# Kernel optimization log

Hardware: AMD Instinct MI355X
Metric: run time of the kernel (lower is better)

Reference implementation:

```python
import jax, jax.numpy as jnp
import numpy as np

ATT_UNITS = 64
DEC_DIM = 512
ENC_DIM = 512


def setup_inputs() -> dict:
    key = jax.random.key(0)
    k1, k2, k3, k4, k5 = jax.random.split(key, 5)
    B, S = 256, 512
    # glorot-uniform-ish init scales
    def glorot(k, shape):
        fan_in, fan_out = shape[0], shape[1]
        lim = np.sqrt(6.0 / (fan_in + fan_out))
        return jax.random.uniform(k, shape, jnp.float32, -lim, lim)
    return {
        "decoder_hidden_state": jax.random.normal(k1, (B, DEC_DIM), jnp.float32),
        "encoder_output": jax.random.normal(k2, (B, S, ENC_DIM), jnp.float32),
        "w1_kernel": glorot(k3, (DEC_DIM, ATT_UNITS)),
        "w1_bias": jnp.zeros((ATT_UNITS,), jnp.float32),
        "w2_kernel": glorot(k4, (ENC_DIM, ATT_UNITS)),
        "w2_bias": jnp.zeros((ATT_UNITS,), jnp.float32),
        "v_kernel": glorot(k5, (ATT_UNITS, 1)),
        "v_bias": jnp.zeros((1,), jnp.float32),
    }


def reference(decoder_hidden_state, encoder_output, w1_kernel, w1_bias,
              w2_kernel, w2_bias, v_kernel, v_bias):
    # dec proj: [B, 1, U]; enc proj: [B, S, U]
    dec = (decoder_hidden_state @ w1_kernel + w1_bias)[:, None, :]
    enc = jnp.einsum('bse,eu->bsu', encoder_output, w2_kernel) + w2_bias
    # score: [B, S, 1]
    score = jnp.tanh(dec + enc) @ v_kernel + v_bias
    att_weights = jax.nn.softmax(score, axis=1)  # softmax over sequence axis
    # weighted sum over S -> [B, E]
    context_vector = jnp.sum(att_weights * encoder_output, axis=1)
    return (context_vector, att_weights)
```

## Files before the change

### kernel.cpp

```cpp
#include <hip/hip_runtime.h>
#include <hip/hip_bf16.h>

constexpr int NB = 256;
constexpr int SQ = 512;
constexpr int ED = 512;
constexpr int DD = 512;
constexpr int UU = 64;
constexpr int NT = 32;

typedef __attribute__((ext_vector_type(8))) short bf16x8;
typedef __attribute__((ext_vector_type(4))) float f32x4;

__device__ __forceinline__ void stage16(const void* g, void* l) {
  __builtin_amdgcn_global_load_lds(
      (const __attribute__((address_space(1))) void*)g,
      (__attribute__((address_space(3))) void*)l, 16, 0, 0);
}

__device__ __forceinline__ unsigned short bf16_rne(float f) {
  unsigned int u = __float_as_uint(f);
  u += 0x7FFFu + ((u >> 16) & 1u);
  return (unsigned short)(u >> 16);
}

__device__ __forceinline__ uint2 split2(float v0, float v1) {
  unsigned int u0 = __float_as_uint(v0), u1 = __float_as_uint(v1);
  unsigned int h0 = u0 & 0xFFFF0000u, h1 = u1 & 0xFFFF0000u;
  unsigned int hi = (u0 >> 16) | h1;
  float r0 = v0 - __uint_as_float(h0);
  float r1 = v1 - __uint_as_float(h1);
  unsigned int lo = (__float_as_uint(r0) >> 16) | (__float_as_uint(r1) & 0xFFFF0000u);
  return make_uint2(hi, lo);
}

constexpr size_t WS_DEC   = 131072;
constexpr size_t WS_LBUF  = 196608;
constexpr size_t WS_CTILE = 262144;

__global__ __launch_bounds__(256) void prep_all(
    const float* __restrict__ w2, unsigned short* __restrict__ wsb,
    const float* __restrict__ dh, const float* __restrict__ w1,
    const float* __restrict__ w1b, const float* __restrict__ w2b,
    float* __restrict__ dec_ws) {
  const int blk = blockIdx.x;
  __shared__ float red[256];
  if (blk < 128) {
    int tid = blk * 256 + threadIdx.x;
    int j    = tid & 7;
    int lane = (tid >> 3) & 63;
    int nt   = (tid >> 9) & 3;
    int ks   = tid >> 11;
    int e = ks * 32 + (lane >> 4) * 8 + j;
    int u = nt * 16 + (lane & 15);
    wsb[tid] = bf16_rne(w2[e * UU + u]);
  } else {
    const int b = blk - 128;
    const int t = threadIdx.x;
    const int wave = t >> 6;
    const float* dhb = dh + (size_t)b * DD;
    const int e0 = wave * 128;
    float s = 0.f;
    #pragma unroll 8
    for (int i = 0; i < 128; ++i) {
      int e = e0 + i;
      s = fmaf(dhb[e], w1[e * UU + (t & 63)], s);
    }
    red[t] = s;
    __syncthreads();
    if (t < 64) {
      float d = w1b[t] + w2b[t] + red[t] + red[64 + t] + red[128 + t] + red[192 + t];
      dec_ws[b * UU + t] = d;
    }
  }
}

__global__ __launch_bounds__(256, 4) void attn_tile(
    const float* __restrict__ x,
    const float* __restrict__ vk,
    const unsigned short* __restrict__ wsb,
    const float* __restrict__ dec_ws,
    float* __restrict__ lbuf,
    float* __restrict__ ctile,
    float* __restrict__ out)
{
  const int bid = blockIdx.x;
  const int b  = bid >> 5;
  const int tl = bid & 31;
  const int t = threadIdx.x;
  const int wave = t >> 6;
  const int lane = t & 63;
  const int ul = lane & 15;
  const int g  = lane >> 4;
  const int swz = (ul & 7) << 4;
  const int kw = wave >> 1;
  const int nw = wave & 1;

  __shared__ __align__(16) unsigned char slab[16][2048];
  __shared__ __align__(16) f32x4 red4[4][64];
  __shared__ float psum[2][16];

  const char* gsrc = (const char*)x + (size_t)(b * SQ + tl * 16) * 2048;

  #pragma unroll
  for (int r = 0; r < 4; ++r) {
    int row = wave * 4 + r;
    #pragma unroll
    for (int h = 0; h < 2; ++h) {
      int off = h * 1024 + lane * 16;
      stage16(gsrc + (size_t)row * 2048 + (size_t)(off ^ ((row & 7) << 4)),
              &slab[row][off]);
    }
  }

  const unsigned short* bp = wsb + lane * 8;
  bf16x8 bf[8][2];
  #pragma unroll
  for (int i = 0; i < 8; ++i) {
    #pragma unroll
    for (int j = 0; j < 2; ++j)
      bf[i][j] = *(const bf16x8*)(bp + (kw * 8 + i) * 2048 + (nw * 2 + j) * 512);
  }
  float dvs[2], vvs[2];
  #pragma unroll
  for (int j = 0; j < 2; ++j) {
    dvs[j] = dec_ws[b * UU + (nw * 2 + j) * 16 + ul];
    vvs[j] = vk[(nw * 2 + j) * 16 + ul];
  }
  float av = fabsf(vk[lane]);
  av += __shfl_xor(av, 1);
  av += __shfl_xor(av, 2);
  av += __shfl_xor(av, 4);
  av += __shfl_xor(av, 8);
  av += __shfl_xor(av, 16);
  av += __shfl_xor(av, 32);
  const float M = av;

  __syncthreads();

  const f32x4 zero4 = {0.f, 0.f, 0.f, 0.f};
  f32x4 acc[2];
  acc[0] = zero4;
  acc[1] = zero4;

  const unsigned char* Ab = &slab[ul][0];
  #pragma unroll
  for (int i = 0; i < 8; ++i) {
    const int k = kw * 8 + i;
    f32x4 a0 = *(const f32x4*)(Ab + ((g * 32 + k * 128) ^ swz));
    f32x4 a1 = *(const f32x4*)(Ab + ((g * 32 + k * 128 + 16) ^ swz));
    uint2 p0 = split2(a0[0], a0[1]);
    uint2 p1 = split2(a0[2], a0[3]);
    uint2 p2 = split2(a1[0], a1[1]);
    uint2 p3 = split2(a1[2], a1[3]);
    unsigned int hiw[4] = {p0.x, p1.x, p2.x, p3.x};
    unsigned int low[4] = {p0.y, p1.y, p2.y, p3.y};
    bf16x8 ahi, alo;
    memcpy(&ahi, hiw, 16);
    memcpy(&alo, low, 16);
    #pragma unroll
    for (int j = 0; j < 2; ++j) {
      acc[j] = __builtin_amdgcn_mfma_f32_16x16x32_bf16(ahi, bf[i][j], acc[j], 0, 0, 0);
      acc[j] = __builtin_amdgcn_mfma_f32_16x16x32_bf16(alo, bf[i][j], acc[j], 0, 0, 0);
    }
  }

  if (kw == 0) {
    red4[nw * 2 + 0][lane] = acc[0];
    red4[nw * 2 + 1][lane] = acc[1];
  }
  __syncthreads();
  if (kw == 1) {
    #pragma unroll
    for (int j = 0; j < 2; ++j) {
      f32x4 o = red4[nw * 2 + j][lane];
      acc[j][0] += o[0];
      acc[j][1] += o[1];
      acc[j][2] += o[2];
      acc[j][3] += o[3];
    }
    #pragma unroll
    for (int r = 0; r < 4; ++r) {
      float s = 0.f;
      #pragma unroll
      for (int j = 0; j < 2; ++j) {
        float z = acc[j][r] + dvs[j];
        float ez = __expf(2.f * z);
        float th = 1.f - 2.f / (ez + 1.f);
        s = fmaf(th, vvs[j], s);
      }
      s += __shfl_xor(s, 1);
      s += __shfl_xor(s, 2);
      s += __shfl_xor(s, 4);
      s += __shfl_xor(s, 8);
      if (ul == 0) psum[nw][g * 4 + r] = s;
    }
  }
  __syncthreads();

  float p[4];
  float lsum = 0.f;
  #pragma unroll
  for (int r = 0; r < 4; ++r) {
    int row = g * 4 + r;
    float sc = psum[0][row] + psum[1][row];
    p[r] = __expf(sc - M);
    lsum += p[r];
  }
  lsum += __shfl_xor(lsum, 16);
  lsum += __shfl_xor(lsum, 32);
  lsum += __shfl_xor(lsum, 1);
  lsum += __shfl_xor(lsum, 2);
  lsum += __shfl_xor(lsum, 4);
  lsum += __shfl_xor(lsum, 8);
  lsum *= 0.0625f;

  if (wave == 0 && ul == 0) {
    float* att = out + (size_t)NB * ED + (size_t)b * SQ + tl * 16;
    #pragma unroll
    for (int r = 0; r < 4; ++r) att[g * 4 + r] = p[r];
  }
  if (t == 0) lbuf[b * NT + tl] = lsum;

  {
    const int cbase = wave * 512 + lane * 8;
    float cx = 0.f, cy = 0.f;
    #pragma unroll
    for (int rr = 0; rr < 16; ++rr) {
      const float2 v = *(const float2*)&slab[rr][cbase ^ ((rr & 7) << 4)];
      float pi = __shfl(p[rr & 3], (rr >> 2) << 4);
      cx = fmaf(pi, v.x, cx);
      cy = fmaf(pi, v.y, cy);
    }
    float* ct = ctile + ((size_t)b * NT + tl) * ED + wave * 128 + lane * 2;
    ct[0] = cx;
    ct[1] = cy;
  }
}

__global__ __launch_bounds__(256) void combine(
    const float* __restrict__ lbuf,
    const float* __restrict__ ctile, float* __restrict__ out) {
  const int b = blockIdx.x;
  const int t = threadIdx.x;

  float L = 0.f;
  #pragma unroll 8
  for (int j = 0; j < NT; ++j) L += lbuf[b * NT + j];
  const float inv = 1.f / L;

  float* att = out + (size_t)NB * ED + (size_t)b * SQ;
  #pragma unroll
  for (int s = t; s < SQ; s += 256) att[s] *= inv;

  const float* ct = ctile + (size_t)b * NT * ED;
  #pragma unroll
  for (int e = t; e < ED; e += 256) {
    float c = 0.f;
    #pragma unroll 8
    for (int j = 0; j < NT; ++j) c += ct[j * ED + e];
    out[(size_t)b * ED + e] = c * inv;
  }
}

extern "C" void kernel_launch(void* const* d_in, const int* in_sizes, int n_in,
                              void* d_out, int out_size, void* d_ws, size_t ws_size,
                              hipStream_t stream) {
  const float* dh  = (const float*)d_in[0];
  const float* x   = (const float*)d_in[1];
  const float* w1  = (const float*)d_in[2];
  const float* w1b = (const float*)d_in[3];
  const float* w2  = (const float*)d_in[4];
  const float* w2b = (const float*)d_in[5];
  const float* vk  = (const float*)d_in[6];
  unsigned short* wsb = (unsigned short*)d_ws;
  float* dec_ws = (float*)((char*)d_ws + WS_DEC);
  float* lbuf   = (float*)((char*)d_ws + WS_LBUF);
  float* ctile  = (float*)((char*)d_ws + WS_CTILE);
  float* out = (float*)d_out;

  prep_all<<<384, 256, 0, stream>>>(w2, wsb, dh, w1, w1b, w2b, dec_ws);
  attn_tile<<<NB * NT, 256, 0, stream>>>(x, vk, wsb, dec_ws, lbuf, ctile, out);
  combine<<<NB, 256, 0, stream>>>(lbuf, ctile, out);
}
```

Baseline: 82.85 us.

## Double attn_tile block to 512 threads with four-way K split per tile

```diff
diff --git a/kernel.cpp b/kernel.cpp
--- a/kernel.cpp
+++ b/kernel.cpp
@@ -74,7 +74,7 @@
   }
 }
 
-__global__ __launch_bounds__(256, 4) void attn_tile(
+__global__ __launch_bounds__(512, 6) void attn_tile(
     const float* __restrict__ x,
     const float* __restrict__ vk,
     const unsigned short* __restrict__ wsb,
@@ -96,14 +96,14 @@
   const int nw = wave & 1;
 
   __shared__ __align__(16) unsigned char slab[16][2048];
-  __shared__ __align__(16) f32x4 red4[4][64];
+  __shared__ __align__(16) f32x4 red4[3][4][64];
   __shared__ float psum[2][16];
 
   const char* gsrc = (const char*)x + (size_t)(b * SQ + tl * 16) * 2048;
 
   #pragma unroll
-  for (int r = 0; r < 4; ++r) {
-    int row = wave * 4 + r;
+  for (int r = 0; r < 2; ++r) {
+    int row = wave * 2 + r;
     #pragma unroll
     for (int h = 0; h < 2; ++h) {
       int off = h * 1024 + lane * 16;
@@ -113,13 +113,11 @@
   }
 
   const unsigned short* bp = wsb + lane * 8;
-  bf16x8 bf[8][2];
-  #pragma unroll
-  for (int i = 0; i < 8; ++i) {
-    #pragma unroll
-    for (int j = 0; j < 2; ++j)
-      bf[i][j] = *(const bf16x8*)(bp + (kw * 8 + i) * 2048 + (nw * 2 + j) * 512);
-  }
+  auto loadB = [&](int k, int j) {
+    return *(const bf16x8*)(bp + k * 2048 + (nw * 2 + j) * 512);
+  };
+  bf16x8 bfc0 = loadB(kw * 4, 0), bfc1 = loadB(kw * 4, 1);
+
   float dvs[2], vvs[2];
   #pragma unroll
   for (int j = 0; j < 2; ++j) {
@@ -144,8 +142,10 @@
 
   const unsigned char* Ab = &slab[ul][0];
   #pragma unroll
-  for (int i = 0; i < 8; ++i) {
-    const int k = kw * 8 + i;
+  for (int i = 0; i < 4; ++i) {
+    const int k = kw * 4 + i;
+    bf16x8 bn0, bn1;
+    if (i < 3) { bn0 = loadB(k + 1, 0); bn1 = loadB(k + 1, 1); }
     f32x4 a0 = *(const f32x4*)(Ab + ((g * 32 + k * 128) ^ swz));
     f32x4 a1 = *(const f32x4*)(Ab + ((g * 32 + k * 128 + 16) ^ swz));
     uint2 p0 = split2(a0[0], a0[1]);
@@ -157,26 +157,30 @@
     bf16x8 ahi, alo;
     memcpy(&ahi, hiw, 16);
     memcpy(&alo, low, 16);
+    acc[0] = __builtin_amdgcn_mfma_f32_16x16x32_bf16(ahi, bfc0, acc[0], 0, 0, 0);
+    acc[0] = __builtin_amdgcn_mfma_f32_16x16x32_bf16(alo, bfc0, acc[0], 0, 0, 0);
+    acc[1] = __builtin_amdgcn_mfma_f32_16x16x32_bf16(ahi, bfc1, acc[1], 0, 0, 0);
+    acc[1] = __builtin_amdgcn_mfma_f32_16x16x32_bf16(alo, bfc1, acc[1], 0, 0, 0);
+    bfc0 = bn0;
+    bfc1 = bn1;
+  }
+
+  if (kw > 0) {
+    red4[kw - 1][nw * 2 + 0][lane] = acc[0];
+    red4[kw - 1][nw * 2 + 1][lane] = acc[1];
+  }
+  __syncthreads();
+  if (kw == 0) {
     #pragma unroll
     for (int j = 0; j < 2; ++j) {
-      acc[j] = __builtin_amdgcn_mfma_f32_16x16x32_bf16(ahi, bf[i][j], acc[j], 0, 0, 0);
-      acc[j] = __builtin_amdgcn_mfma_f32_16x16x32_bf16(alo, bf[i][j], acc[j], 0, 0, 0);
-    }
-  }
-
-  if (kw == 0) {
-    red4[nw * 2 + 0][lane] = acc[0];
-    red4[nw * 2 + 1][lane] = acc[1];
-  }
-  __syncthreads();
-  if (kw == 1) {
-    #pragma unroll
-    for (int j = 0; j < 2; ++j) {
-      f32x4 o = red4[nw * 2 + j][lane];
-      acc[j][0] += o[0];
-      acc[j][1] += o[1];
-      acc[j][2] += o[2];
-      acc[j][3] += o[3];
+      const int s = nw * 2 + j;
+      f32x4 o0 = red4[0][s][lane];
+      f32x4 o1 = red4[1][s][lane];
+      f32x4 o2 = red4[2][s][lane];
+      acc[j][0] += o0[0] + o1[0] + o2[0];
+      acc[j][1] += o0[1] + o1[1] + o2[1];
+      acc[j][2] += o0[2] + o1[2] + o2[2];
+      acc[j][3] += o0[3] + o1[3] + o2[3];
     }
     #pragma unroll
     for (int r = 0; r < 4; ++r) {
@@ -222,18 +226,15 @@
   if (t == 0) lbuf[b * NT + tl] = lsum;
 
   {
-    const int cbase = wave * 512 + lane * 8;
-    float cx = 0.f, cy = 0.f;
+    const int cbase = wave * 256 + lane * 4;
+    float cx = 0.f;
     #pragma unroll
     for (int rr = 0; rr < 16; ++rr) {
-      const float2 v = *(const float2*)&slab[rr][cbase ^ ((rr & 7) << 4)];
+      const float v = *(const float*)&slab[rr][cbase ^ ((rr & 7) << 4)];
       float pi = __shfl(p[rr & 3], (rr >> 2) << 4);
-      cx = fmaf(pi, v.x, cx);
-      cy = fmaf(pi, v.y, cy);
-    }
-    float* ct = ctile + ((size_t)b * NT + tl) * ED + wave * 128 + lane * 2;
-    ct[0] = cx;
-    ct[1] = cy;
+      cx = fmaf(pi, v, cx);
+    }
+    ctile[((size_t)b * NT + tl) * ED + wave * 64 + lane] = cx;
   }
 }
 
@@ -279,6 +280,6 @@
   float* out = (float*)d_out;
 
   prep_all<<<384, 256, 0, stream>>>(w2, wsb, dh, w1, w1b, w2b, dec_ws);
-  attn_tile<<<NB * NT, 256, 0, stream>>>(x, vk, wsb, dec_ws, lbuf, ctile, out);
+  attn_tile<<<NB * NT, 512, 0, stream>>>(x, vk, wsb, dec_ws, lbuf, ctile, out);
   combine<<<NB, 256, 0, stream>>>(lbuf, ctile, out);
 }
```

Result: slower. 97.06 us (+17.1%).
